# Kernel optimization log

Measured on AMD Instinct MI355X. Metric: run time of the kernel, lower is better.

The kernel has to match this reference:

```python
import jax, jax.numpy as jnp
import numpy as np

B, C, D, H, W = 4, 1, 128, 192, 192


def setup_inputs() -> dict:
    key = jax.random.key(0)
    ks = jax.random.split(key, 8)
    x = jax.random.normal(ks[0], (B, C, D, H, W), jnp.float32)
    y = jax.random.normal(ks[1], (B, C, H, W), jnp.float32)
    rot_0 = jax.random.normal(ks[2], (B, 1), jnp.float32) * 0.1
    rot_1 = jax.random.normal(ks[3], (B, 1), jnp.float32) * 0.1
    rot_2 = jax.random.normal(ks[4], (B, 1), jnp.float32) * 0.1
    trans_1 = jax.random.normal(ks[5], (B, 1), jnp.float32) * 0.05
    trans_2 = jax.random.normal(ks[6], (B, 1), jnp.float32) * 0.05
    center_point = (jnp.tile(jnp.array([[D / 2., H / 2., W / 2.]], jnp.float32), (B, 1))
                    + jax.random.normal(ks[7], (B, 3), jnp.float32))
    return {"x": x, "y": y, "rot_0": rot_0, "rot_1": rot_1, "rot_2": rot_2,
            "trans_1": trans_1, "trans_2": trans_2, "center_point": center_point}


def _euler2mat(a):
    # a: [B,3] angles (z, y, x), ZYX intrinsic composition as in source
    z, y, x = a[:, 0], a[:, 1], a[:, 2]
    cz, sz = jnp.cos(z), jnp.sin(z)
    cy, sy = jnp.cos(y), jnp.sin(y)
    cx, sx = jnp.cos(x), jnp.sin(x)
    o = jnp.ones_like(z)
    zr = jnp.zeros_like(z)
    zmat = jnp.stack([cz, -sz, zr, sz, cz, zr, zr, zr, o], 1).reshape(-1, 3, 3)
    ymat = jnp.stack([cy, zr, sy, zr, o, zr, -sy, zr, cy], 1).reshape(-1, 3, 3)
    xmat = jnp.stack([o, zr, zr, zr, cx, -sx, zr, sx, cx], 1).reshape(-1, 3, 3)
    return zmat @ ymat @ xmat


def _rigid4x4(rot3, t):
    # rot3: [B,3,3], t: [B,3] -> [B,4,4]
    bn = rot3.shape[0]
    top = jnp.concatenate([rot3, t[:, :, None]], axis=-1)          # [B,3,4]
    bot = jnp.broadcast_to(jnp.array([[[0., 0., 0., 1.]]], jnp.float32), (bn, 1, 4))
    return jnp.concatenate([top, bot], axis=1)


def _trans_mat(t):
    bn = t.shape[0]
    eye = jnp.broadcast_to(jnp.eye(3, dtype=jnp.float32), (bn, 3, 3))
    return _rigid4x4(eye, t)


def _affine_grid(mat, shape):
    # mat: [B,4,4]; voxel-coordinate grid (nitorch convention): g = R @ c + t
    d, h, w = shape
    zz, yy, xx = jnp.meshgrid(jnp.arange(d, dtype=jnp.float32),
                              jnp.arange(h, dtype=jnp.float32),
                              jnp.arange(w, dtype=jnp.float32), indexing='ij')
    coords = jnp.stack([zz, yy, xx], axis=-1)                      # [D,H,W,3]
    return (jnp.einsum('dhwj,bij->bdhwi', coords, mat[:, :3, :3])
            + mat[:, None, None, None, :3, 3])                    # [B,D,H,W,3]


def _grid_pull_one(vol, g):
    # vol: [C,D,H,W]; g: [D,H,W,3] voxel coords; trilinear, zero boundary
    d, h, w = vol.shape[1], vol.shape[2], vol.shape[3]
    g0f = jnp.floor(g)
    frac = g - g0f
    g0 = g0f.astype(jnp.int32)
    out = jnp.zeros((vol.shape[0],) + g.shape[:-1], vol.dtype)
    for dz in (0, 1):
        wz = frac[..., 0] if dz else 1. - frac[..., 0]
        iz = g0[..., 0] + dz
        for dy in (0, 1):
            wy = frac[..., 1] if dy else 1. - frac[..., 1]
            iy = g0[..., 1] + dy
            for dx in (0, 1):
                wx = frac[..., 2] if dx else 1. - frac[..., 2]
                ix = g0[..., 2] + dx
                valid = ((iz >= 0) & (iz < d) & (iy >= 0) & (iy < h)
                         & (ix >= 0) & (ix < w)).astype(vol.dtype)
                v = vol[:, jnp.clip(iz, 0, d - 1), jnp.clip(iy, 0, h - 1),
                        jnp.clip(ix, 0, w - 1)]                   # [C,D,H,W]
                out = out + v * (wz * wy * wx * valid)[None]
    return out


def reference(x, y, rot_0, rot_1, rot_2, trans_1, trans_2, center_point):
    d, h, w = x.shape[2], x.shape[3], x.shape[4]
    t1 = _trans_mat(-center_point)
    t2 = _trans_mat(center_point)
    # first translation component is detached*0 -> exact zeros
    trans = jnp.concatenate([jnp.zeros_like(trans_1), trans_1 * h, trans_2 * w], axis=1)
    angles = jnp.concatenate([rot_0, rot_1, rot_2], axis=1)
    rot = _euler2mat(angles)
    rigid = _rigid4x4(rot, trans)
    mat = t2 @ (rigid @ t1)                                        # center-about-point rigid
    grid = _affine_grid(mat, (d, h, w))                            # [B,D,H,W,3]
    x_warp = jax.vmap(_grid_pull_one)(x, grid)                     # [B,C,D,H,W]
    x_2d = jnp.mean(x_warp, axis=2)                                # [B,C,H,W]
    return (x_2d, x_warp, y)
```

## Files before the change

kernel.cpp:

```cpp
#include <hip/hip_runtime.h>

#define Bn 4
#define Dd 128
#define Hh 192
#define Ww 192

#define PLANE (Hh * Ww)
#define VOL   (Dd * PLANE)
#define N2D   (Bn * PLANE)
#define WARP_OFF ((size_t)N2D)
#define Y_OFF (WARP_OFF + (size_t)Bn * VOL)

#define DT 8
#define HT 8
#define WT 32
#define NDB (Dd / DT)
#define NHB (Hh / HT)
#define NWB (Ww / WT)
#define NBLK (Bn * NDB * NHB * NWB)
#define NCH NDB

#define SZ 17
#define SY 16
#define SXP 48
#define ZSTRIDE (SY * SXP)
#define LDSF (SZ * ZSTRIDE)

typedef float f2 __attribute__((ext_vector_type(2)));
typedef f2 __attribute__((aligned(4))) f2u;
__device__ __forceinline__ f2 load2(const float* p) { return *(const f2u*)p; }

__device__ __forceinline__ void gload_lds16(const float* g, float* l) {
    __builtin_amdgcn_global_load_lds(
        (const __attribute__((address_space(1))) void*)g,
        (__attribute__((address_space(3))) void*)l,
        16, 0, 0);
}

__global__ __launch_bounds__(256) void tbl_kernel(const float* __restrict__ rot0,
                                                  const float* __restrict__ rot1,
                                                  const float* __restrict__ rot2,
                                                  const float* __restrict__ tr1,
                                                  const float* __restrict__ tr2,
                                                  const float* __restrict__ cp,
                                                  float* __restrict__ tbl) {
    const int id = blockIdx.x * 256 + threadIdx.x;
    if (id >= NBLK) return;
    const int wblk = id % NWB;
    const int t1   = id / NWB;
    const int hblk = t1 % NHB;
    const int t2   = t1 / NHB;
    const int dblk = t2 & (NDB - 1);
    const int b    = t2 >> 4;

    const float z = rot0[b], y = rot1[b], x = rot2[b];
    const float cz = cosf(z), sz = sinf(z);
    const float cy = cosf(y), sy = sinf(y);
    const float cx = cosf(x), sx = sinf(x);
    const float A0 = cz * cy;
    const float B0 = -sz * cx + cz * sy * sx;
    const float C0 = sz * sx + cz * sy * cx;
    const float A1 = sz * cy;
    const float B1 = cz * cx + sz * sy * sx;
    const float C1 = -cz * sx + sz * sy * cx;
    const float A2 = -sy;
    const float B2 = cy * sx;
    const float C2 = cy * cx;
    const float c0 = cp[b * 3 + 0], c1 = cp[b * 3 + 1], c2 = cp[b * 3 + 2];
    const float E0 = -(A0 * c0 + B0 * c1 + C0 * c2) + c0;
    const float E1 = -(A1 * c0 + B1 * c1 + C1 * c2) + tr1[b] * (float)Hh + c1;
    const float E2 = -(A2 * c0 + B2 * c1 + C2 * c2) + tr2[b] * (float)Ww + c2;

    const int d0 = dblk * DT, h0 = hblk * HT, w0 = wblk * WT;
    const float dlo = (float)d0, dhi = (float)(d0 + DT - 1);
    const float hlo = (float)h0, hhi = (float)(h0 + HT - 1);
    const float wlo = (float)w0, whi = (float)(w0 + WT - 1);

    const float loZ = E0 + fminf(A0 * dlo, A0 * dhi) + fminf(B0 * hlo, B0 * hhi) + fminf(C0 * wlo, C0 * whi);
    const float hiZ = E0 + fmaxf(A0 * dlo, A0 * dhi) + fmaxf(B0 * hlo, B0 * hhi) + fmaxf(C0 * wlo, C0 * whi);
    const float loY = E1 + fminf(A1 * dlo, A1 * dhi) + fminf(B1 * hlo, B1 * hhi) + fminf(C1 * wlo, C1 * whi);
    const float hiY = E1 + fmaxf(A1 * dlo, A1 * dhi) + fmaxf(B1 * hlo, B1 * hhi) + fmaxf(C1 * wlo, C1 * whi);
    const float loX = E2 + fminf(A2 * dlo, A2 * dhi) + fminf(B2 * hlo, B2 * hhi) + fminf(C2 * wlo, C2 * whi);
    const float hiX = E2 + fmaxf(A2 * dlo, A2 * dhi) + fmaxf(B2 * hlo, B2 * hhi) + fmaxf(C2 * wlo, C2 * whi);

    const int lz = max(0, min((int)floorf(loZ) - 1, Dd - 1));
    const int hz = min(Dd - 1, (int)floorf(hiZ) + 2);
    const int ly = max(0, (int)floorf(loY) - 1);
    const int hy = min(Hh - 1, (int)floorf(hiY) + 2);
    const int lx = max(0, (int)floorf(loX) - 1);
    const int lx4 = lx & ~3;
    const int hx = min(Ww - 2, (int)floorf(hiX) + 2);

    const int hzrel = max(0, hz - lz);
    const bool fits = (hzrel <= SZ - 1) && (hy - ly <= SY - 1) && (hx - lx4 <= SXP - 2);
    const bool interior = (loZ >= 0.01f) && (hiZ < (float)(Dd - 1) - 0.01f) &&
                          (loY >= 0.01f) && (hiY < (float)(Hh - 1) - 0.01f) &&
                          (loX >= 0.01f) && (hiX < (float)(Ww - 1) - 0.01f);

    const float bz = E0 + A0 * dlo + B0 * hlo + C0 * wlo - (float)lz;
    const float by = E1 + A1 * dlo + B1 * hlo + C1 * wlo - (float)ly;
    const float bx = E2 + A2 * dlo + B2 * hlo + C2 * wlo - (float)lx4;

    float* T = tbl + (size_t)id * 16;
    T[0] = A0; T[1] = B0; T[2]  = C0; T[3]  = bz;
    T[4] = A1; T[5] = B1; T[6]  = C1; T[7]  = by;
    T[8] = A2; T[9] = B2; T[10] = C2; T[11] = bx;
    int* TI = (int*)T;
    TI[12] = lz; TI[13] = ly; TI[14] = lx4;
    TI[15] = (fits ? 1 : 0) | (interior ? 2 : 0) |
             (b << 2) | (dblk << 4) | (hblk << 8) | (wblk << 13) | (hzrel << 16);
}

template <bool WP>
__global__ __launch_bounds__(256) void warp_tiled(const float* __restrict__ x,
                                                  const float* __restrict__ tbl,
                                                  float* __restrict__ out,
                                                  float* __restrict__ partial) {
    __shared__ __align__(16) float box[LDSF];

    const int g  = blockIdx.x;
    const int wl = (g & 7) * (NBLK / 8) + (g >> 3);

    const float4* T4 = (const float4*)(tbl + (size_t)wl * 16);
    const float4 r0 = T4[0], r1 = T4[1], r2 = T4[2];
    const int4   r3 = ((const int4*)T4)[3];
    const int lz = r3.x, ly = r3.y, lx4 = r3.z, fl = r3.w;
    const bool fits = fl & 1, interior = fl & 2;
    const int b     = (fl >> 2) & 3;
    const int dblk  = (fl >> 4) & 15;
    const int hblk  = (fl >> 8) & 31;
    const int wblk  = (fl >> 13) & 7;
    const int hzrel = (fl >> 16) & 31;
    const int d0 = dblk * DT, h0 = hblk * HT, w0 = wblk * WT;

    const float A0 = r0.x, B0 = r0.y, C0 = r0.z, bz = r0.w;
    const float A1 = r1.x, B1 = r1.y, C1 = r1.z, by = r1.w;
    const float A2 = r2.x, B2 = r2.y, C2 = r2.z, bx = r2.w;

    const int t = threadIdx.x;
    const int w_in = t & 31;
    const int h_in = t >> 5;
    const int lane = t & 63;
    const int wid  = t >> 6;

    const float fh = (float)h_in, fw = (float)w_in;
    const float fz0 = bz + B0 * fh + C0 * fw;
    const float fy0 = by + B1 * fh + C1 * fw;
    const float fx0 = bx + B2 * fh + C2 * fw;

    const float* __restrict__ V = x + (size_t)b * VOL;
    float* __restrict__ obase = out + WARP_OFF + (size_t)b * VOL +
                                (size_t)d0 * PLANE + (size_t)(h0 + h_in) * Ww + (w0 + w_in);

    float sum = 0.0f;

    if (fits) {
        const int r0i = lane / 12,             c0i = (lane - r0i * 12) * 4;
        const int i1  = 64 + lane;  const int r1i = i1 / 12, c1i = (i1 - r1i * 12) * 4;
        const int i2  = 128 + lane; const int r2i = i2 / 12, c2i = (i2 - r2i * 12) * 4;
        const int off0 = min(ly + r0i, Hh - 1) * Ww + min(lx4 + c0i, Ww - 4);
        const int off1 = min(ly + r1i, Hh - 1) * Ww + min(lx4 + c1i, Ww - 4);
        const int off2 = min(ly + r2i, Hh - 1) * Ww + min(lx4 + c2i, Ww - 4);

        for (int z = wid; z <= hzrel; z += 4) {
            const float* Vz = V + (size_t)min(lz + z, Dd - 1) * PLANE;
            float* Lz = box + z * ZSTRIDE;
            gload_lds16(Vz + off0, Lz);
            gload_lds16(Vz + off1, Lz + 256);
            gload_lds16(Vz + off2, Lz + 512);
        }
        __syncthreads();

        if (interior) {
            #pragma unroll
            for (int j = 0; j < DT; ++j) {
                const float fd = (float)j;
                const float gz = fmaf(A0, fd, fz0);
                const float gy = fmaf(A1, fd, fy0);
                const float gx = fmaf(A2, fd, fx0);
                const float fz = floorf(gz), fy = floorf(gy), fx = floorf(gx);
                const float tz = gz - fz, ty = gy - fy, tx = gx - fx;
                const int izr = (int)fz, iyr = (int)fy, ixr = (int)fx;
                const int base = izr * ZSTRIDE + iyr * SXP + ixr;

                const f2 qa = load2(&box[base]);
                const f2 qb = load2(&box[base + SXP]);
                const f2 qc = load2(&box[base + ZSTRIDE]);
                const f2 qd = load2(&box[base + ZSTRIDE + SXP]);

                const float wx0 = 1.0f - tx, wy0 = 1.0f - ty, wz0 = 1.0f - tz;
                const float v00 = fmaf(wx0, qa.x, tx * qa.y);
                const float v01 = fmaf(wx0, qb.x, tx * qb.y);
                const float v10 = fmaf(wx0, qc.x, tx * qc.y);
                const float v11 = fmaf(wx0, qd.x, tx * qd.y);
                const float vz0 = fmaf(wy0, v00, ty * v01);
                const float vz1 = fmaf(wy0, v10, ty * v11);
                const float val = fmaf(wz0, vz0, tz * vz1);

                __builtin_nontemporal_store(val, obase + (size_t)j * PLANE);
                sum += val;
            }
        } else {
            const float fz0a = fz0 + (float)lz;
            const float fy0a = fy0 + (float)ly;
            const float fx0a = fx0 + (float)lx4;
            #pragma unroll
            for (int j = 0; j < DT; ++j) {
                const float fd = (float)j;
                const float gz = fmaf(A0, fd, fz0a);
                const float gy = fmaf(A1, fd, fy0a);
                const float gx = fmaf(A2, fd, fx0a);

                const float fz = floorf(gz), fy = floorf(gy), fx = floorf(gx);
                const float tz = gz - fz, ty = gy - fy, tx = gx - fx;
                const int iz = (int)fz, iy = (int)fy, ix = (int)fx;

                const float wz0 = ((unsigned)iz       < (unsigned)Dd) ? (1.0f - tz) : 0.0f;
                const float wz1 = ((unsigned)(iz + 1) < (unsigned)Dd) ? tz : 0.0f;
                const float wy0 = ((unsigned)iy       < (unsigned)Hh) ? (1.0f - ty) : 0.0f;
                const float wy1 = ((unsigned)(iy + 1) < (unsigned)Hh) ? ty : 0.0f;
                const float wx0 = ((unsigned)ix       < (unsigned)Ww) ? (1.0f - tx) : 0.0f;
                const float wx1 = ((unsigned)(ix + 1) < (unsigned)Ww) ? tx : 0.0f;

                const bool right  = (ix >= Ww - 1);
                const bool leftok = (ix >= 0);
                const float WL = (right ? 0.0f : wx0) + (leftok ? 0.0f : wx1);
                const float WH = (right ? wx0 : 0.0f) + (leftok ? wx1 : 0.0f);

                const int zc0 = min(max(iz, 0), Dd - 1) - lz;
                const int zc1 = min(max(iz + 1, 0), Dd - 1) - lz;
                const int yc0 = min(max(iy, 0), Hh - 1) - ly;
                const int yc1 = min(max(iy + 1, 0), Hh - 1) - ly;
                const int ixl = min(max(ix, 0), Ww - 2);
                const int col = max(ixl - lx4, 0);

                const int b00 = max(zc0, 0) * ZSTRIDE + max(yc0, 0) * SXP + col;
                const int b01 = max(zc0, 0) * ZSTRIDE + max(yc1, 0) * SXP + col;
                const int b10 = max(zc1, 0) * ZSTRIDE + max(yc0, 0) * SXP + col;
                const int b11 = max(zc1, 0) * ZSTRIDE + max(yc1, 0) * SXP + col;

                const f2 qa = load2(&box[min(b00, LDSF - 2)]);
                const f2 qb = load2(&box[min(b01, LDSF - 2)]);
                const f2 qc = load2(&box[min(b10, LDSF - 2)]);
                const f2 qd = load2(&box[min(b11, LDSF - 2)]);

                const float v00 = fmaf(WL, qa.x, WH * qa.y);
                const float v01 = fmaf(WL, qb.x, WH * qb.y);
                const float v10 = fmaf(WL, qc.x, WH * qc.y);
                const float v11 = fmaf(WL, qd.x, WH * qd.y);

                const float vz0 = fmaf(wy0, v00, wy1 * v01);
                const float vz1 = fmaf(wy0, v10, wy1 * v11);
                const float val = fmaf(wz0, vz0, wz1 * vz1);

                __builtin_nontemporal_store(val, obase + (size_t)j * PLANE);
                sum += val;
            }
        }
    } else {
        const float fz0a = fz0 + (float)lz;
        const float fy0a = fy0 + (float)ly;
        const float fx0a = fx0 + (float)lx4;
        #pragma unroll
        for (int j = 0; j < DT; ++j) {
            const float fd = (float)j;
            const float gz = fmaf(A0, fd, fz0a);
            const float gy = fmaf(A1, fd, fy0a);
            const float gx = fmaf(A2, fd, fx0a);

            const float fz = floorf(gz), fy = floorf(gy), fx = floorf(gx);
            const float tz = gz - fz, ty = gy - fy, tx = gx - fx;
            const int iz = (int)fz, iy = (int)fy, ix = (int)fx;

            const float wz0 = ((unsigned)iz       < (unsigned)Dd) ? (1.0f - tz) : 0.0f;
            const float wz1 = ((unsigned)(iz + 1) < (unsigned)Dd) ? tz : 0.0f;
            const float wy0 = ((unsigned)iy       < (unsigned)Hh) ? (1.0f - ty) : 0.0f;
            const float wy1 = ((unsigned)(iy + 1) < (unsigned)Hh) ? ty : 0.0f;
            const float wx0 = ((unsigned)ix       < (unsigned)Ww) ? (1.0f - tx) : 0.0f;
            const float wx1 = ((unsigned)(ix + 1) < (unsigned)Ww) ? tx : 0.0f;

            const bool right  = (ix >= Ww - 1);
            const bool leftok = (ix >= 0);
            const float WL = (right ? 0.0f : wx0) + (leftok ? 0.0f : wx1);
            const float WH = (right ? wx0 : 0.0f) + (leftok ? wx1 : 0.0f);

            const int iz0c = min(max(iz, 0), Dd - 1);
            const int iz1c = min(max(iz + 1, 0), Dd - 1);
            const int iy0c = min(max(iy, 0), Hh - 1);
            const int iy1c = min(max(iy + 1, 0), Hh - 1);
            const int ixl  = min(max(ix, 0), Ww - 2);

            const f2 q00 = load2(V + (size_t)iz0c * PLANE + iy0c * Ww + ixl);
            const f2 q01 = load2(V + (size_t)iz0c * PLANE + iy1c * Ww + ixl);
            const f2 q10 = load2(V + (size_t)iz1c * PLANE + iy0c * Ww + ixl);
            const f2 q11 = load2(V + (size_t)iz1c * PLANE + iy1c * Ww + ixl);

            const float v00 = fmaf(WL, q00.x, WH * q00.y);
            const float v01 = fmaf(WL, q01.x, WH * q01.y);
            const float v10 = fmaf(WL, q10.x, WH * q10.y);
            const float v11 = fmaf(WL, q11.x, WH * q11.y);

            const float vz0 = fmaf(wy0, v00, wy1 * v01);
            const float vz1 = fmaf(wy0, v10, wy1 * v11);
            const float val = fmaf(wz0, vz0, wz1 * vz1);

            __builtin_nontemporal_store(val, obase + (size_t)j * PLANE);
            sum += val;
        }
    }

    if (WP) {
        partial[((size_t)(b * NCH + dblk) * Hh + (h0 + h_in)) * Ww + (w0 + w_in)] = sum;
    }
}

__global__ __launch_bounds__(256) void reduce_kernel(const float* __restrict__ partial,
                                                     const float* __restrict__ yin,
                                                     float* __restrict__ out) {
    const int idx = blockIdx.x * 256 + threadIdx.x;
    if (idx >= N2D) return;
    const int b = idx / PLANE;
    const int rem = idx - b * PLANE;
    const float* p = partial + (size_t)b * NCH * PLANE + rem;
    float s = 0.0f;
    #pragma unroll
    for (int c = 0; c < NCH; ++c) s += p[(size_t)c * PLANE];
    out[idx] = s * (1.0f / (float)Dd);
    out[Y_OFF + idx] = yin[idx];
}

__global__ __launch_bounds__(256) void reduce_fallback_kernel(const float* __restrict__ yin,
                                                              float* __restrict__ out) {
    const int idx = blockIdx.x * 256 + threadIdx.x;
    if (idx >= N2D) return;
    const int b = idx / PLANE;
    const int rem = idx - b * PLANE;
    const float* p = out + WARP_OFF + (size_t)b * VOL + rem;
    float s = 0.0f;
    #pragma unroll 8
    for (int d = 0; d < Dd; ++d) s += p[(size_t)d * PLANE];
    out[idx] = s * (1.0f / (float)Dd);
    out[Y_OFF + idx] = yin[idx];
}

extern "C" void kernel_launch(void* const* d_in, const int* in_sizes, int n_in,
                              void* d_out, int out_size, void* d_ws, size_t ws_size,
                              hipStream_t stream) {
    const float* x    = (const float*)d_in[0];
    const float* yin  = (const float*)d_in[1];
    const float* rot0 = (const float*)d_in[2];
    const float* rot1 = (const float*)d_in[3];
    const float* rot2 = (const float*)d_in[4];
    const float* tr1  = (const float*)d_in[5];
    const float* tr2  = (const float*)d_in[6];
    const float* cp   = (const float*)d_in[7];

    float* tbl = (float*)d_ws;
    float* partial = tbl + (size_t)NBLK * 16;
    const size_t need = ((size_t)NBLK * 16 + (size_t)Bn * NCH * PLANE) * sizeof(float);

    tbl_kernel<<<(NBLK + 255) / 256, 256, 0, stream>>>(rot0, rot1, rot2, tr1, tr2, cp, tbl);

    if (ws_size >= need) {
        warp_tiled<true><<<NBLK, 256, 0, stream>>>(x, tbl, (float*)d_out, partial);
        reduce_kernel<<<(N2D + 255) / 256, 256, 0, stream>>>(partial, yin, (float*)d_out);
    } else {
        warp_tiled<false><<<NBLK, 256, 0, stream>>>(x, tbl, (float*)d_out, partial);
        reduce_fallback_kernel<<<(N2D + 255) / 256, 256, 0, stream>>>(yin, (float*)d_out);
    }
}
```

Measured before the change: 56.44 us.

## Double depth tile to 16 with 512-thread blocks sharing one LDS box

Doubles the depth tile so each block stages a taller LDS box of 25 z-slices and covers it with 512 threads split into two depth halves. Adjacent depth sub-tiles now share one box, so the overlapping halo slices are loaded once instead of twice. The sampling index and weight computation is moved ahead of the barrier so it overlaps the async global-to-LDS loads. The trade-off is larger LDS per block (about 77KB), which may lower occupancy, and fewer blocks in the grid.

```diff
diff --git a/kernel.cpp b/kernel.cpp
--- a/kernel.cpp
+++ b/kernel.cpp
@@ -11,16 +11,16 @@
 #define WARP_OFF ((size_t)N2D)
 #define Y_OFF (WARP_OFF + (size_t)Bn * VOL)
 
-#define DT 8
+#define DT 16
 #define HT 8
 #define WT 32
 #define NDB (Dd / DT)
 #define NHB (Hh / HT)
 #define NWB (Ww / WT)
 #define NBLK (Bn * NDB * NHB * NWB)
-#define NCH NDB
-
-#define SZ 17
+#define NCH (NDB * 2)
+
+#define SZ 25
 #define SY 16
 #define SXP 48
 #define ZSTRIDE (SY * SXP)
@@ -51,7 +51,7 @@
     const int hblk = t1 % NHB;
     const int t2   = t1 / NHB;
     const int dblk = t2 & (NDB - 1);
-    const int b    = t2 >> 4;
+    const int b    = t2 >> 3;
 
     const float z = rot0[b], y = rot1[b], x = rot2[b];
     const float cz = cosf(z), sz = sinf(z);
@@ -108,11 +108,11 @@
     int* TI = (int*)T;
     TI[12] = lz; TI[13] = ly; TI[14] = lx4;
     TI[15] = (fits ? 1 : 0) | (interior ? 2 : 0) |
-             (b << 2) | (dblk << 4) | (hblk << 8) | (wblk << 13) | (hzrel << 16);
+             (b << 2) | (dblk << 4) | (hblk << 7) | (wblk << 12) | (hzrel << 15);
 }
 
 template <bool WP>
-__global__ __launch_bounds__(256) void warp_tiled(const float* __restrict__ x,
+__global__ __launch_bounds__(512) void warp_tiled(const float* __restrict__ x,
                                                   const float* __restrict__ tbl,
                                                   float* __restrict__ out,
                                                   float* __restrict__ partial) {
@@ -127,10 +127,10 @@
     const int lz = r3.x, ly = r3.y, lx4 = r3.z, fl = r3.w;
     const bool fits = fl & 1, interior = fl & 2;
     const int b     = (fl >> 2) & 3;
-    const int dblk  = (fl >> 4) & 15;
-    const int hblk  = (fl >> 8) & 31;
-    const int wblk  = (fl >> 13) & 7;
-    const int hzrel = (fl >> 16) & 31;
+    const int dblk  = (fl >> 4) & 7;
+    const int hblk  = (fl >> 7) & 31;
+    const int wblk  = (fl >> 12) & 7;
+    const int hzrel = (fl >> 15) & 127;
     const int d0 = dblk * DT, h0 = hblk * HT, w0 = wblk * WT;
 
     const float A0 = r0.x, B0 = r0.y, C0 = r0.z, bz = r0.w;
@@ -139,18 +139,20 @@
 
     const int t = threadIdx.x;
     const int w_in = t & 31;
-    const int h_in = t >> 5;
+    const int h_in = (t >> 5) & 7;
+    const int dq   = t >> 8;
     const int lane = t & 63;
     const int wid  = t >> 6;
 
-    const float fh = (float)h_in, fw = (float)w_in;
-    const float fz0 = bz + B0 * fh + C0 * fw;
-    const float fy0 = by + B1 * fh + C1 * fw;
-    const float fx0 = bx + B2 * fh + C2 * fw;
+    const float fh = (float)h_in, fw = (float)w_in, fdq = (float)(dq * 8);
+    const float fz0 = bz + B0 * fh + C0 * fw + A0 * fdq;
+    const float fy0 = by + B1 * fh + C1 * fw + A1 * fdq;
+    const float fx0 = bx + B2 * fh + C2 * fw + A2 * fdq;
 
     const float* __restrict__ V = x + (size_t)b * VOL;
     float* __restrict__ obase = out + WARP_OFF + (size_t)b * VOL +
-                                (size_t)d0 * PLANE + (size_t)(h0 + h_in) * Ww + (w0 + w_in);
+                                (size_t)(d0 + dq * 8) * PLANE +
+                                (size_t)(h0 + h_in) * Ww + (w0 + w_in);
 
     float sum = 0.0f;
 
@@ -162,32 +164,38 @@
         const int off1 = min(ly + r1i, Hh - 1) * Ww + min(lx4 + c1i, Ww - 4);
         const int off2 = min(ly + r2i, Hh - 1) * Ww + min(lx4 + c2i, Ww - 4);
 
-        for (int z = wid; z <= hzrel; z += 4) {
+        for (int z = wid; z <= hzrel; z += 8) {
             const float* Vz = V + (size_t)min(lz + z, Dd - 1) * PLANE;
             float* Lz = box + z * ZSTRIDE;
             gload_lds16(Vz + off0, Lz);
             gload_lds16(Vz + off1, Lz + 256);
             gload_lds16(Vz + off2, Lz + 512);
         }
-        __syncthreads();
 
         if (interior) {
+            int   basev[8];
+            float txv[8], tyv[8], tzv[8];
             #pragma unroll
-            for (int j = 0; j < DT; ++j) {
+            for (int j = 0; j < 8; ++j) {
                 const float fd = (float)j;
                 const float gz = fmaf(A0, fd, fz0);
                 const float gy = fmaf(A1, fd, fy0);
                 const float gx = fmaf(A2, fd, fx0);
                 const float fz = floorf(gz), fy = floorf(gy), fx = floorf(gx);
-                const float tz = gz - fz, ty = gy - fy, tx = gx - fx;
-                const int izr = (int)fz, iyr = (int)fy, ixr = (int)fx;
-                const int base = izr * ZSTRIDE + iyr * SXP + ixr;
-
+                tzv[j] = gz - fz; tyv[j] = gy - fy; txv[j] = gx - fx;
+                basev[j] = (int)fz * ZSTRIDE + (int)fy * SXP + (int)fx;
+            }
+            __syncthreads();
+
+            #pragma unroll
+            for (int j = 0; j < 8; ++j) {
+                const int base = basev[j];
                 const f2 qa = load2(&box[base]);
                 const f2 qb = load2(&box[base + SXP]);
                 const f2 qc = load2(&box[base + ZSTRIDE]);
                 const f2 qd = load2(&box[base + ZSTRIDE + SXP]);
 
+                const float tx = txv[j], ty = tyv[j], tz = tzv[j];
                 const float wx0 = 1.0f - tx, wy0 = 1.0f - ty, wz0 = 1.0f - tz;
                 const float v00 = fmaf(wx0, qa.x, tx * qa.y);
                 const float v01 = fmaf(wx0, qb.x, tx * qb.y);
@@ -201,11 +209,12 @@
                 sum += val;
             }
         } else {
+            __syncthreads();
             const float fz0a = fz0 + (float)lz;
             const float fy0a = fy0 + (float)ly;
             const float fx0a = fx0 + (float)lx4;
             #pragma unroll
-            for (int j = 0; j < DT; ++j) {
+            for (int j = 0; j < 8; ++j) {
                 const float fd = (float)j;
                 const float gz = fmaf(A0, fd, fz0a);
                 const float gy = fmaf(A1, fd, fy0a);
@@ -261,8 +270,8 @@
         const float fz0a = fz0 + (float)lz;
         const float fy0a = fy0 + (float)ly;
         const float fx0a = fx0 + (float)lx4;
-        #pragma unroll
-        for (int j = 0; j < DT; ++j) {
+        #pragma unroll 4
+        for (int j = 0; j < 8; ++j) {
             const float fd = (float)j;
             const float gz = fmaf(A0, fd, fz0a);
             const float gy = fmaf(A1, fd, fy0a);
@@ -310,7 +319,8 @@
     }
 
     if (WP) {
-        partial[((size_t)(b * NCH + dblk) * Hh + (h0 + h_in)) * Ww + (w0 + w_in)] = sum;
+        const int ch = dblk * 2 + dq;
+        partial[((size_t)(b * NCH + ch) * Hh + (h0 + h_in)) * Ww + (w0 + w_in)] = sum;
     }
 }
 
@@ -362,10 +372,10 @@
     tbl_kernel<<<(NBLK + 255) / 256, 256, 0, stream>>>(rot0, rot1, rot2, tr1, tr2, cp, tbl);
 
     if (ws_size >= need) {
-        warp_tiled<true><<<NBLK, 256, 0, stream>>>(x, tbl, (float*)d_out, partial);
+        warp_tiled<true><<<NBLK, 512, 0, stream>>>(x, tbl, (float*)d_out, partial);
         reduce_kernel<<<(N2D + 255) / 256, 256, 0, stream>>>(partial, yin, (float*)d_out);
     } else {
-        warp_tiled<false><<<NBLK, 256, 0, stream>>>(x, tbl, (float*)d_out, partial);
+        warp_tiled<false><<<NBLK, 512, 0, stream>>>(x, tbl, (float*)d_out, partial);
         reduce_fallback_kernel<<<(N2D + 255) / 256, 256, 0, stream>>>(yin, (float*)d_out);
     }
 }
```

Result: faster. 54.40 us (-3.6%).
